# Optimization experiments

Hardware: AMD Instinct MI355X
Metric: run time of the kernel (lower is better)

## Reference

```python
import jax, jax.numpy as jnp
import numpy as np

N, K, D = 131072, 1024, 128
COMMITMENT_COST = 0.25


def setup_inputs() -> dict:
    key = jax.random.key(0)
    k1, k2 = jax.random.split(key)
    c_input = jax.random.normal(k1, (N, D), dtype=jnp.float32)
    # nn.Embedding weight initialized N(0, 0.1)
    embedding_weight = jax.random.normal(k2, (K, D), dtype=jnp.float32) * 0.1
    return {"c_input": c_input, "embedding_weight": embedding_weight}


def reference(c_input, embedding_weight):
    distances = (
        jnp.sum(c_input ** 2, axis=1, keepdims=True)
        + jnp.sum(embedding_weight ** 2, axis=1)
        - 2.0 * jnp.matmul(c_input, embedding_weight.T)
    )
    encoding_indices = jnp.argmin(distances, axis=1)  # [N]
    encodings = jax.nn.one_hot(encoding_indices, K, dtype=c_input.dtype)  # [N, K]
    # one-hot @ weight == direct gather
    quantized = embedding_weight[encoding_indices]  # [N, D]
    e_latent_loss = jnp.mean((jax.lax.stop_gradient(quantized) - c_input) ** 2)
    q_latent_loss = jnp.mean((quantized - jax.lax.stop_gradient(c_input)) ** 2)
    loss = q_latent_loss + COMMITMENT_COST * e_latent_loss
    # straight-through estimator
    quantized_st = c_input + jax.lax.stop_gradient(quantized - c_input)
    return (loss, quantized_st, encodings)
```

## Files before the change

### kernel.cpp

```cpp
#include <hip/hip_runtime.h>
#include <hip/hip_bf16.h>

#define NROWS 131072
#define KC 1024
#define DD 128
#define MARGIN 1e-3f

typedef __attribute__((ext_vector_type(8))) short short8;
typedef __attribute__((ext_vector_type(4))) float f32x4;
typedef __attribute__((ext_vector_type(2))) float f32x2;

__device__ inline short f2bf_hi(float f) {
  unsigned u = __builtin_bit_cast(unsigned, f);
  u += 0x7fffu + ((u >> 16) & 1u);
  return (short)(u >> 16);
}
__device__ inline float bf2f(short s) {
  unsigned u = ((unsigned)(unsigned short)s) << 16;
  return __builtin_bit_cast(float, u);
}

__global__ void vq_prep(const float* __restrict__ E, short* __restrict__ EH,
                        short* __restrict__ EL, float* __restrict__ SE,
                        float* __restrict__ out) {
  int b = blockIdx.x, t = threadIdx.x;
  if (b < 64) {
    int idx = b * 256 + t;
    int s = (idx >> 6) & 3, l = idx & 63;
    int c = idx >> 8;
    int q = l >> 4, n = l & 15;
    const float* src = E + (16 * c + n) * DD + 32 * s + 8 * q;
    short8 h, lo;
#pragma unroll
    for (int j = 0; j < 8; ++j) {
      float x = src[j];
      short hb = f2bf_hi(x);
      h[j] = hb;
      lo[j] = f2bf_hi(x - bf2f(hb));
    }
    *(short8*)(EH + idx * 8) = h;
    *(short8*)(EL + idx * 8) = lo;
  } else {
    if (t == 0) out[0] = 0.f;
    for (int k = t; k < KC; k += 256) {
      double acc = 0.0;
      const float* er = E + k * DD;
      for (int i = 0; i < DD; ++i) { double v = (double)er[i]; acc += v * v; }
      SE[k] = (float)acc;
    }
  }
}

__global__ __launch_bounds__(256, 2) void vq_main(
    const float* __restrict__ X, const float* __restrict__ E,
    const short* __restrict__ EH, const short* __restrict__ EL,
    const float* __restrict__ SE, float* __restrict__ out) {
  __shared__ __align__(16) short lbh[8192];
  __shared__ __align__(16) short lbl[8192];
  __shared__ __align__(16) float lse[KC];
  __shared__ int lidx[128];
  __shared__ int lflag[128];
  __shared__ int lany;
  __shared__ float lx[128];
  __shared__ float lrv[4];
  __shared__ int lri[4];
  __shared__ float lsx;
  __shared__ float lloss[4];

  const int tid = threadIdx.x;
  const int w = tid >> 6, l = tid & 63, q = l >> 4, n = l & 15;
  const int row_base = blockIdx.x * 128;
  const int rot = blockIdx.x & 15;
  const int encb = 1 + NROWS * DD;
  if (tid == 0) lany = 0;
  *(f32x4*)(lse + tid * 4) = *(const f32x4*)(SE + tid * 4);

  float* zb = out + encb + row_base * KC;
  if (tid < 3) __builtin_nontemporal_store(0.f, zb + tid);
  else if (tid == 3) __builtin_nontemporal_store(0.f, zb + 131071);
  float* zb4 = zb + 3;

  short8 ah[2][4], al[2][4];
#pragma unroll
  for (int mt = 0; mt < 2; ++mt) {
    const float* xp = X + (row_base + 32 * w + 16 * mt + n) * DD + 8 * q;
#pragma unroll
    for (int s = 0; s < 4; ++s) {
      f32x4 x0 = *(const f32x4*)(xp + 32 * s);
      f32x4 x1 = *(const f32x4*)(xp + 32 * s + 4);
#pragma unroll
      for (int j = 0; j < 4; ++j) {
        short hb = f2bf_hi(x0[j]);
        ah[mt][s][j] = hb;
        al[mt][s][j] = f2bf_hi(x0[j] - bf2f(hb));
        short hb2 = f2bf_hi(x1[j]);
        ah[mt][s][j + 4] = hb2;
        al[mt][s][j + 4] = f2bf_hi(x1[j] - bf2f(hb2));
      }
    }
  }

  float bestv[8], secv[8];
  int besti[8];
#pragma unroll
  for (int i = 0; i < 8; ++i) { bestv[i] = -3e38f; secv[i] = -3e38f; besti[i] = 0; }

  const f32x4 z4 = {0.f, 0.f, 0.f, 0.f};
  for (int cc = 0; cc < 16; ++cc) {
    const int ccr = (cc + rot) & 15;
    {
      const short8* gh = (const short8*)(EH + ccr * 8192);
      const short8* gl = (const short8*)(EL + ccr * 8192);
      short8* dh = (short8*)lbh;
      short8* dl = (short8*)lbl;
#pragma unroll
      for (int i = 0; i < 4; ++i) {
        int u = i * 256 + tid;
        dh[u] = gh[u];
        dl[u] = gl[u];
      }
    }
    __syncthreads();

#pragma unroll
    for (int u2 = 0; u2 < 8; ++u2) {
      int j = cc * 2048 + u2 * 256 + tid;
      if (j < 32767) __builtin_nontemporal_store(z4, (f32x4*)(zb4 + 4 * j));
    }
    __builtin_amdgcn_sched_barrier(0);

#pragma unroll
    for (int nt = 0; nt < 4; ++nt) {
      f32x4 a0 = {0.f, 0.f, 0.f, 0.f}, a1 = {0.f, 0.f, 0.f, 0.f};
#pragma unroll
      for (int s = 0; s < 4; ++s) {
        short8 bh  = *(const short8*)(lbh + ((nt * 4 + s) * 64 + l) * 8);
        short8 blo = *(const short8*)(lbl + ((nt * 4 + s) * 64 + l) * 8);
        a0 = __builtin_amdgcn_mfma_f32_16x16x32_bf16(ah[0][s], bh,  a0, 0, 0, 0);
        a1 = __builtin_amdgcn_mfma_f32_16x16x32_bf16(ah[1][s], bh,  a1, 0, 0, 0);
        a0 = __builtin_amdgcn_mfma_f32_16x16x32_bf16(al[0][s], bh,  a0, 0, 0, 0);
        a1 = __builtin_amdgcn_mfma_f32_16x16x32_bf16(al[1][s], bh,  a1, 0, 0, 0);
        a0 = __builtin_amdgcn_mfma_f32_16x16x32_bf16(ah[0][s], blo, a0, 0, 0, 0);
        a1 = __builtin_amdgcn_mfma_f32_16x16x32_bf16(ah[1][s], blo, a1, 0, 0, 0);
      }
      int k = ccr * 64 + nt * 16 + n;
      float hse = 0.5f * lse[k];
#pragma unroll
      for (int r = 0; r < 4; ++r) {
        {
          float sc = a0[r] - hse;
          bool gt = sc > bestv[r];
          secv[r] = gt ? bestv[r] : fmaxf(secv[r], sc);
          if (gt) { bestv[r] = sc; besti[r] = k; }
        }
        {
          int sl = 4 + r;
          float sc = a1[r] - hse;
          bool gt = sc > bestv[sl];
          secv[sl] = gt ? bestv[sl] : fmaxf(secv[sl], sc);
          if (gt) { bestv[sl] = sc; besti[sl] = k; }
        }
      }
    }
    __syncthreads();
  }

#pragma unroll
  for (int slot = 0; slot < 8; ++slot) {
    float v = bestv[slot], s2 = secv[slot];
    int bi = besti[slot];
#pragma unroll
    for (int m = 1; m <= 8; m <<= 1) {
      float v2 = __shfl_xor(v, m, 64);
      float sv2 = __shfl_xor(s2, m, 64);
      int i2 = __shfl_xor(bi, m, 64);
      float ns = fmaxf(fminf(v, v2), fmaxf(s2, sv2));
      if (v2 > v || (v2 == v && i2 < bi)) { v = v2; bi = i2; }
      s2 = ns;
    }
    if (n == 0) {
      int mt = slot >> 2, r = slot & 3;
      int rl = 32 * w + 16 * mt + 4 * q + r;
      int f = (v - s2) <= MARGIN;
      lidx[rl] = bi;
      lflag[rl] = f;
      if (f) lany = 1;
    }
  }
  __syncthreads();

  if (lany) {
    for (int rl = 0; rl < 128; ++rl) {
      if (lflag[rl] == 0) continue;
      if (tid < DD) lx[tid] = X[(row_base + rl) * DD + tid];
      __syncthreads();
      if (tid < 64) {
        double v0 = lx[tid], v1 = lx[tid + 64];
        double s = v0 * v0 + v1 * v1;
#pragma unroll
        for (int m = 1; m < 64; m <<= 1) s += __shfl_xor(s, m, 64);
        if (tid == 0) lsx = (float)s;
      }
      __syncthreads();
      float dmin = 3e38f; int kmin = 0;
      for (int kk = tid; kk < KC; kk += 256) {
        double dot = 0.0;
        const float* er = E + kk * DD;
        for (int i = 0; i < DD; ++i) dot += (double)lx[i] * (double)er[i];
        float a = lsx + lse[kk];
        float b2 = (float)(2.0 * dot);
        float dnp = a - b2;
        if (dnp < dmin) { dmin = dnp; kmin = kk; }
      }
#pragma unroll
      for (int m = 1; m < 64; m <<= 1) {
        float v2 = __shfl_xor(dmin, m, 64);
        int k2 = __shfl_xor(kmin, m, 64);
        if (v2 < dmin || (v2 == dmin && k2 < kmin)) { dmin = v2; kmin = k2; }
      }
      if (l == 0) { lrv[w] = dmin; lri[w] = kmin; }
      __syncthreads();
      if (tid == 0) {
        float dm = lrv[0]; int km = lri[0];
#pragma unroll
        for (int t2 = 1; t2 < 4; ++t2)
          if (lrv[t2] < dm || (lrv[t2] == dm && lri[t2] < km)) { dm = lrv[t2]; km = lri[t2]; }
        lidx[rl] = km;
      }
      __syncthreads();
    }
  }
  __syncthreads();

  float lp = 0.f;
  for (int rl = w; rl < 128; rl += 4) {
    int row = row_base + rl;
    int idx = lidx[rl];
    f32x2 xv = *(const f32x2*)(X + row * DD + 2 * l);
    f32x2 ev = *(const f32x2*)(E + idx * DD + 2 * l);
    float d0 = ev[0] - xv[0], d1 = ev[1] - xv[1];
    __builtin_nontemporal_store(xv[0] + d0, out + 1 + row * DD + 2 * l);
    __builtin_nontemporal_store(xv[1] + d1, out + 1 + row * DD + 2 * l + 1);
    lp += d0 * d0 + d1 * d1;
    if (l == (idx & 63)) out[encb + row * KC + idx] = 1.f;
  }
#pragma unroll
  for (int m = 1; m < 64; m <<= 1) lp += __shfl_xor(lp, m, 64);
  if (l == 0) lloss[w] = lp;
  __syncthreads();
  if (tid == 0) {
    float t = (lloss[0] + lloss[1] + lloss[2] + lloss[3]) *
              (1.25f / ((float)NROWS * (float)DD));
    atomicAdd(out, t);
  }
}

extern "C" void kernel_launch(void* const* d_in, const int* in_sizes, int n_in,
                              void* d_out, int out_size, void* d_ws, size_t ws_size,
                              hipStream_t stream) {
  const float* X = (const float*)d_in[0];
  const float* E = (const float*)d_in[1];
  float* out = (float*)d_out;
  short* EH = (short*)d_ws;
  short* EL = EH + KC * DD;
  float* SE = (float*)(EL + KC * DD);
  vq_prep<<<65, 256, 0, stream>>>(E, EH, EL, SE, out);
  vq_main<<<NROWS / 128, 256, 0, stream>>>(X, E, EH, EL, SE, out);
}
```

Baseline: 763.1 us.

## Double-buffer codebook chunks in LDS with register prefetch

Loads the next codebook chunk from global memory into registers while the MFMA work on the current LDS buffer runs, then writes it to the alternate LDS buffer. This removes one barrier per chunk and hides global load latency. It also drops the per-block chunk rotation. It doubles LDS use for the chunk buffers and adds register pressure.

```diff
diff --git a/kernel.cpp b/kernel.cpp
--- a/kernel.cpp
+++ b/kernel.cpp
@@ -55,8 +55,8 @@
     const float* __restrict__ X, const float* __restrict__ E,
     const short* __restrict__ EH, const short* __restrict__ EL,
     const float* __restrict__ SE, float* __restrict__ out) {
-  __shared__ __align__(16) short lbh[8192];
-  __shared__ __align__(16) short lbl[8192];
+  __shared__ __align__(16) short lbh[2][8192];
+  __shared__ __align__(16) short lbl[2][8192];
   __shared__ __align__(16) float lse[KC];
   __shared__ int lidx[128];
   __shared__ int lflag[128];
@@ -70,7 +70,6 @@
   const int tid = threadIdx.x;
   const int w = tid >> 6, l = tid & 63, q = l >> 4, n = l & 15;
   const int row_base = blockIdx.x * 128;
-  const int rot = blockIdx.x & 15;
   const int encb = 1 + NROWS * DD;
   if (tid == 0) lany = 0;
   *(f32x4*)(lse + tid * 4) = *(const f32x4*)(SE + tid * 4);
@@ -105,37 +104,49 @@
 #pragma unroll
   for (int i = 0; i < 8; ++i) { bestv[i] = -3e38f; secv[i] = -3e38f; besti[i] = 0; }
 
+  {
+    const short8* gh = (const short8*)(EH);
+    const short8* gl = (const short8*)(EL);
+    short8* dh = (short8*)lbh[0];
+    short8* dl = (short8*)lbl[0];
+#pragma unroll
+    for (int i = 0; i < 4; ++i) {
+      int u = i * 256 + tid;
+      dh[u] = gh[u];
+      dl[u] = gl[u];
+    }
+  }
+  __syncthreads();
+
   const f32x4 z4 = {0.f, 0.f, 0.f, 0.f};
   for (int cc = 0; cc < 16; ++cc) {
-    const int ccr = (cc + rot) & 15;
-    {
-      const short8* gh = (const short8*)(EH + ccr * 8192);
-      const short8* gl = (const short8*)(EL + ccr * 8192);
-      short8* dh = (short8*)lbh;
-      short8* dl = (short8*)lbl;
+    const int cur = cc & 1;
+
+    short8 sh[4], sl[4];
+    if (cc < 15) {
+      const short8* gh = (const short8*)(EH + (cc + 1) * 8192);
+      const short8* gl = (const short8*)(EL + (cc + 1) * 8192);
 #pragma unroll
       for (int i = 0; i < 4; ++i) {
         int u = i * 256 + tid;
-        dh[u] = gh[u];
-        dl[u] = gl[u];
-      }
-    }
-    __syncthreads();
+        sh[i] = gh[u];
+        sl[i] = gl[u];
+      }
+    }
 
 #pragma unroll
     for (int u2 = 0; u2 < 8; ++u2) {
       int j = cc * 2048 + u2 * 256 + tid;
       if (j < 32767) __builtin_nontemporal_store(z4, (f32x4*)(zb4 + 4 * j));
     }
-    __builtin_amdgcn_sched_barrier(0);
 
 #pragma unroll
     for (int nt = 0; nt < 4; ++nt) {
       f32x4 a0 = {0.f, 0.f, 0.f, 0.f}, a1 = {0.f, 0.f, 0.f, 0.f};
 #pragma unroll
       for (int s = 0; s < 4; ++s) {
-        short8 bh  = *(const short8*)(lbh + ((nt * 4 + s) * 64 + l) * 8);
-        short8 blo = *(const short8*)(lbl + ((nt * 4 + s) * 64 + l) * 8);
+        short8 bh  = *(const short8*)(&lbh[cur][((nt * 4 + s) * 64 + l) * 8]);
+        short8 blo = *(const short8*)(&lbl[cur][((nt * 4 + s) * 64 + l) * 8]);
         a0 = __builtin_amdgcn_mfma_f32_16x16x32_bf16(ah[0][s], bh,  a0, 0, 0, 0);
         a1 = __builtin_amdgcn_mfma_f32_16x16x32_bf16(ah[1][s], bh,  a1, 0, 0, 0);
         a0 = __builtin_amdgcn_mfma_f32_16x16x32_bf16(al[0][s], bh,  a0, 0, 0, 0);
@@ -143,7 +154,7 @@
         a0 = __builtin_amdgcn_mfma_f32_16x16x32_bf16(ah[0][s], blo, a0, 0, 0, 0);
         a1 = __builtin_amdgcn_mfma_f32_16x16x32_bf16(ah[1][s], blo, a1, 0, 0, 0);
       }
-      int k = ccr * 64 + nt * 16 + n;
+      int k = cc * 64 + nt * 16 + n;
       float hse = 0.5f * lse[k];
 #pragma unroll
       for (int r = 0; r < 4; ++r) {
@@ -154,12 +165,23 @@
           if (gt) { bestv[r] = sc; besti[r] = k; }
         }
         {
-          int sl = 4 + r;
+          int sl2 = 4 + r;
           float sc = a1[r] - hse;
-          bool gt = sc > bestv[sl];
-          secv[sl] = gt ? bestv[sl] : fmaxf(secv[sl], sc);
-          if (gt) { bestv[sl] = sc; besti[sl] = k; }
+          bool gt = sc > bestv[sl2];
+          secv[sl2] = gt ? bestv[sl2] : fmaxf(secv[sl2], sc);
+          if (gt) { bestv[sl2] = sc; besti[sl2] = k; }
         }
+      }
+    }
+
+    if (cc < 15) {
+      short8* dh = (short8*)lbh[cur ^ 1];
+      short8* dl = (short8*)lbl[cur ^ 1];
+#pragma unroll
+      for (int i = 0; i < 4; ++i) {
+        int u = i * 256 + tid;
+        dh[u] = sh[i];
+        dl[u] = sl[i];
       }
     }
     __syncthreads();
```

Result: no change. 775.2 us (+1.6%).
